# Optimization experiments

Measured on AMD Instinct MI355X. Metric: run time of the kernel, lower is better.

Reference implementation:

```python
import jax, jax.numpy as jnp
import numpy as np
from jax import lax

B, C, H, W = 16, 256, 128, 128
MAX_ROOMS = 10

def _conv(x, w, b):
    y = lax.conv_general_dilated(x, w, window_strides=(1, 1), padding='SAME',
                                 dimension_numbers=('NCHW', 'OIHW', 'NCHW'))
    return y + b[None, :, None, None]

def setup_inputs() -> dict:
    key = jax.random.key(0)
    ks = jax.random.split(key, 16)
    def w(k, shape, fan_in):
        return jax.random.normal(k, shape, jnp.float32) * (1.0 / np.sqrt(fan_in))
    inp = {
        'features': jax.random.normal(ks[0], (B, C, H, W), jnp.float32),
        'conv1_w': w(ks[1], (C // 2, C, 3, 3), C * 9),
        'conv1_b': jnp.zeros((C // 2,), jnp.float32),
        'conv2_w': w(ks[2], (MAX_ROOMS, C // 2, 3, 3), (C // 2) * 9),
        'conv2_b': jnp.zeros((MAX_ROOMS,), jnp.float32),
        'lin1_w': w(ks[3], (256, C * 64), C * 64),
        'lin1_b': jnp.zeros((256,), jnp.float32),
        'lin2_w': w(ks[4], (128, 256), 256),
        'lin2_b': jnp.zeros((128,), jnp.float32),
        'adj1_w': w(ks[5], (64, 256), 256),
        'adj1_b': jnp.zeros((64,), jnp.float32),
        'adj2_w': w(ks[6], (32, 64), 64),
        'adj2_b': jnp.zeros((32,), jnp.float32),
        'adj3_w': w(ks[7], (1, 32), 32),
        'adj3_b': jnp.zeros((1,), jnp.float32),
    }
    return inp

def reference(features, conv1_w, conv1_b, conv2_w, conv2_b,
              lin1_w, lin1_b, lin2_w, lin2_b,
              adj1_w, adj1_b, adj2_w, adj2_b, adj3_w, adj3_b):
    # room detector: conv -> relu -> conv -> sigmoid
    h = jax.nn.relu(_conv(features, conv1_w, conv1_b))
    room_maps = jax.nn.sigmoid(_conv(h, conv2_w, conv2_b))  # [B, max_rooms, H, W]

    # room features: adaptive avg pool to 8x8 (exact since H,W divisible by 8)
    b, c = features.shape[0], features.shape[1]
    pooled = features.reshape(b, c, 8, H // 8, 8, W // 8).mean(axis=(3, 5))  # [B,C,8,8]
    flat = pooled.reshape(b, c * 64)
    feat = jax.nn.relu(flat @ lin1_w.T + lin1_b) @ lin2_w.T + lin2_b  # [B,128]

    # adjacency: original loop uses the SAME pair_feat=cat([feat,feat]) for every (i,j),
    # so compute one prob per batch row and broadcast to all off-diagonal entries.
    pair = jnp.concatenate([feat, feat], axis=-1)  # [B,256]
    a = jax.nn.relu(pair @ adj1_w.T + adj1_b)
    a = jax.nn.relu(a @ adj2_w.T + adj2_b)
    p = jax.nn.sigmoid(a @ adj3_w.T + adj3_b)  # [B,1]
    off_diag = 1.0 - jnp.eye(MAX_ROOMS, dtype=features.dtype)
    adjacency = p[:, :, None] * off_diag[None]  # [B, max_rooms, max_rooms]

    return room_maps, feat, adjacency
```

## Files before the change

### kernel.cpp

```cpp
#include <hip/hip_runtime.h>

#define HH 128
#define WW 128
#define FEAT_OFF 2621440ull
#define ADJ_OFF  2623488ull

typedef __bf16 bf16x8 __attribute__((ext_vector_type(8)));
typedef float  f32x4  __attribute__((ext_vector_type(4)));

__device__ __forceinline__ unsigned short f2bf(float f) {
  unsigned int u = __float_as_uint(f);
  unsigned int r = ((u >> 16) & 1u) + 0x7fffu;
  return (unsigned short)((u + r) >> 16);
}
__device__ __forceinline__ void gl_lds16(const void* g, void* l) {
  __builtin_amdgcn_global_load_lds((const __attribute__((address_space(1))) unsigned int*)g,
                                   (__attribute__((address_space(3))) unsigned int*)l, 16, 0, 0);
}
__device__ __forceinline__ int SW(int r) { return (r ^ (r >> 2)) & 3; }

#define FENCE() asm volatile("" ::: "memory")
#define BARRIER() do { FENCE(); __builtin_amdgcn_s_barrier(); FENCE(); } while (0)
#define LBAR() do { asm volatile("s_waitcnt lgkmcnt(0)" ::: "memory"); __builtin_amdgcn_s_barrier(); FENCE(); } while (0)

__global__ void prep_kernel(const float* __restrict__ w1, const float* __restrict__ w2,
                            unsigned short* __restrict__ W1t, unsigned short* __restrict__ W2t,
                            unsigned short* __restrict__ zp) {
  int id = blockIdx.x * 256 + threadIdx.x;
  if (id < 2048) zp[id] = 0;
  if (id < 294912) {
    int ci = id & 255, co = (id >> 8) & 127, dxy = id >> 15;
    int dy = dxy / 3, dx = dxy - 3 * dy;
    W1t[id] = f2bf(w1[((co * 256 + ci) * 3 + dy) * 3 + dx]);
  }
  if (id < 18432) {
    int ci = id & 127, co = (id >> 7) & 15, dxy = id >> 11;
    int dy = dxy / 3, dx = dxy - 3 * dy;
    W2t[id] = (co < 10) ? f2bf(w2[((co * 128 + ci) * 3 + dy) * 3 + dx]) : (unsigned short)0;
  }
}

__global__ void nhwc_kernel(const float* __restrict__ F, unsigned short* __restrict__ Xn) {
  int t = threadIdx.x, bi = blockIdx.x;
  int x = t & 127;
  int cg = ((bi & 7) << 1) | (t >> 7);
  int y = (bi >> 3) & 127;
  int b = bi >> 10;
  const float* src = F + (((size_t)(b * 256 + cg * 16)) * HH + y) * WW + x;
  __align__(16) unsigned short v[16];
#pragma unroll
  for (int i = 0; i < 16; ++i) v[i] = f2bf(src[(size_t)i * (HH * WW)]);
  unsigned short* dst = Xn + ((((size_t)b * HH + y) * WW) + x) * 256 + cg * 16;
  *(uint4*)dst = *(const uint4*)&v[0];
  *(uint4*)(dst + 8) = *(const uint4*)&v[8];
}

__global__ __launch_bounds__(512) void conv1_kernel(const unsigned short* __restrict__ X,
                                                    const unsigned short* __restrict__ Wt,
                                                    const float* __restrict__ bias,
                                                    unsigned short* __restrict__ Hout,
                                                    const unsigned short* __restrict__ zp) {
  extern __shared__ __align__(16) unsigned short smem[];
  const int t = threadIdx.x, l = t & 63, w = t >> 6;
  int bid = (blockIdx.x & 7) * 128 + (blockIdx.x >> 3);
  const int b = bid >> 6, y0 = (bid & 63) * 2;
  const int ko = l >> 4, r0 = l & 15;
  const int wr = w >> 1, wc = w & 1;
  const int ir = wr >> 1, xoff = (wr & 1) * 64;

  f32x4 acc[4][4];
#pragma unroll
  for (int i = 0; i < 4; ++i)
#pragma unroll
    for (int j = 0; j < 4; ++j) acc[i][j] = {0.f, 0.f, 0.f, 0.f};

  auto stage = [&](int p, int bufsel) {
    int dy = p >> 3, cb = p & 7;
    unsigned short* buf = smem + bufsel * 21504;
    for (int j = w; j < 18; j += 8) {
      int air = (j >= 9) ? 1 : 0;
      int jj = j - air * 9;
      int er = jj * 16 + (l >> 2);
      int xin = er - 1;
      int row = y0 - 1 + dy + air;
      const unsigned short* g;
      if (row >= 0 && row < HH && xin >= 0 && xin < WW && er < 130) {
        int kq = (l & 3) ^ SW(er);
        g = X + (((size_t)b * HH + row) * WW + xin) * 256 + cb * 32 + kq * 8;
      } else g = zp + l * 8;
      gl_lds16(g, buf + j * 512);
    }
    for (int j = w; j < 24; j += 8) {
      int dxi = j >> 3, jj = j & 7;
      int co = jj * 16 + (l >> 2);
      int kq = (l & 3) ^ SW(co);
      gl_lds16(Wt + (((size_t)(dy * 3 + dxi)) * 128 + co) * 256 + cb * 32 + kq * 8,
               buf + 9216 + j * 512);
    }
  };

  stage(0, 0);
  for (int p = 0; p < 24; ++p) {
    if (p < 23) {
      stage(p + 1, (p + 1) & 1);
      FENCE();
      asm volatile("s_waitcnt vmcnt(5)" ::: "memory");
    } else {
      FENCE();
      asm volatile("s_waitcnt vmcnt(0)" ::: "memory");
    }
    BARRIER();
    const unsigned short* buf = smem + (p & 1) * 21504;
    const unsigned short* Ab = buf + ir * 4608;
    const unsigned short* Bb = buf + 9216;
#pragma unroll
    for (int dx = 0; dx < 3; ++dx) {
      bf16x8 a[4], bb[4];
#pragma unroll
      for (int mf = 0; mf < 4; ++mf) {
        int er = xoff + mf * 16 + r0 + dx;
        a[mf] = *(const bf16x8*)(Ab + er * 32 + ((ko ^ SW(er)) << 3));
      }
#pragma unroll
      for (int nf = 0; nf < 4; ++nf) {
        int co = wc * 64 + nf * 16 + r0;
        bb[nf] = *(const bf16x8*)(Bb + dx * 4096 + co * 32 + ((ko ^ SW(co)) << 3));
      }
#pragma unroll
      for (int mf = 0; mf < 4; ++mf)
#pragma unroll
        for (int nf = 0; nf < 4; ++nf)
          acc[mf][nf] = __builtin_amdgcn_mfma_f32_16x16x32_bf16(a[mf], bb[nf], acc[mf][nf], 0, 0, 0);
    }
    BARRIER();
  }

  unsigned short* Ebuf = smem;
  for (int c = 0; c < 4; ++c) {
    if (wr == c) {
#pragma unroll
      for (int nf = 0; nf < 4; ++nf) {
        int col = wc * 64 + nf * 16 + r0;
        float bv = bias[col];
#pragma unroll
        for (int mf = 0; mf < 4; ++mf)
#pragma unroll
          for (int j = 0; j < 4; ++j) {
            int rloc = mf * 16 + (l >> 4) * 4 + j;
            Ebuf[rloc * 128 + col] = f2bf(fmaxf(acc[mf][nf][j] + bv, 0.f));
          }
      }
    }
    LBAR();
    size_t base = (((size_t)b * HH + (y0 + (c >> 1))) * WW + (c & 1) * 64) * 128;
    ((uint4*)(Hout + base))[t] = ((const uint4*)Ebuf)[t];
    ((uint4*)(Hout + base))[t + 512] = ((const uint4*)Ebuf)[t + 512];
    LBAR();
  }
}

__global__ __launch_bounds__(256) void conv2_kernel(const unsigned short* __restrict__ Hn,
                                                    const unsigned short* __restrict__ Wt,
                                                    const float* __restrict__ bias,
                                                    float* __restrict__ rmaps,
                                                    const unsigned short* __restrict__ zp) {
  extern __shared__ __align__(16) unsigned short smem[];
  const int t = threadIdx.x, l = t & 63, w = t >> 6;
  int bid = (blockIdx.x & 7) * 256 + (blockIdx.x >> 3);
  const int b = bid >> 7, y = bid & 127;
  const int ko = l >> 4, r0 = l & 15;

  f32x4 acc[2];
  acc[0] = {0.f, 0.f, 0.f, 0.f};
  acc[1] = {0.f, 0.f, 0.f, 0.f};

  auto stage = [&](int cb, int bufsel) {
    unsigned short* buf = smem + bufsel * 18432;
    for (int j = w; j < 27; j += 4) {
      int rr = (j >= 18) ? 2 : ((j >= 9) ? 1 : 0);
      int jj = j - rr * 9;
      int er = jj * 16 + (l >> 2);
      int xin = er - 1;
      int row = y - 1 + rr;
      const unsigned short* g;
      if (row >= 0 && row < HH && xin >= 0 && xin < WW && er < 130) {
        int kq = (l & 3) ^ SW(er);
        g = Hn + (((size_t)b * HH + row) * WW + xin) * 128 + cb * 32 + kq * 8;
      } else g = zp + l * 8;
      gl_lds16(g, buf + j * 512);
    }
    for (int j = w; j < 9; j += 4) {
      int co = l >> 2;
      int kq = (l & 3) ^ SW(co);
      gl_lds16(Wt + ((size_t)j * 16 + co) * 128 + cb * 32 + kq * 8, buf + 13824 + j * 512);
    }
  };

  stage(0, 0);
  for (int p = 0; p < 4; ++p) {
    if (p < 3) {
      stage(p + 1, (p + 1) & 1);
      FENCE();
      asm volatile("s_waitcnt vmcnt(8)" ::: "memory");
    } else {
      FENCE();
      asm volatile("s_waitcnt vmcnt(0)" ::: "memory");
    }
    BARRIER();
    const unsigned short* buf = smem + (p & 1) * 18432;
#pragma unroll
    for (int dy = 0; dy < 3; ++dy)
#pragma unroll
      for (int dx = 0; dx < 3; ++dx) {
        int tap = dy * 3 + dx;
        bf16x8 bb = *(const bf16x8*)(buf + 13824 + tap * 512 + r0 * 32 + ((ko ^ SW(r0)) << 3));
#pragma unroll
        for (int mf = 0; mf < 2; ++mf) {
          int er = w * 32 + mf * 16 + r0 + dx;
          bf16x8 a = *(const bf16x8*)(buf + dy * 4608 + er * 32 + ((ko ^ SW(er)) << 3));
          acc[mf] = __builtin_amdgcn_mfma_f32_16x16x32_bf16(a, bb, acc[mf], 0, 0, 0);
        }
      }
    BARRIER();
  }

  float* Ef = (float*)smem;
  float bv = (r0 < 10) ? bias[r0] : 0.f;
#pragma unroll
  for (int mf = 0; mf < 2; ++mf)
#pragma unroll
    for (int j = 0; j < 4; ++j) {
      int x = w * 32 + mf * 16 + (l >> 4) * 4 + j;
      Ef[r0 * 128 + x] = 1.f / (1.f + __expf(-(acc[mf][j] + bv)));
    }
  LBAR();
  {
    int co = t >> 5, xi = (t & 31) * 4;
    *(float4*)&rmaps[(((size_t)b * 10 + co) * HH + y) * WW + xi] = *(float4*)&Ef[co * 128 + xi];
    if (t < 64) {
      int idx = t + 256;
      co = idx >> 5; xi = (idx & 31) * 4;
      *(float4*)&rmaps[(((size_t)b * 10 + co) * HH + y) * WW + xi] = *(float4*)&Ef[co * 128 + xi];
    }
  }
}

__global__ void pool2_kernel(const unsigned short* __restrict__ Xn, float* __restrict__ pooled) {
  int t = threadIdx.x, bi = blockIdx.x;
  int b = bi >> 6, py = (bi >> 3) & 7, px = bi & 7;
  int p = t & 127, half = t >> 7;
  float s0 = 0.f, s1 = 0.f;
  const unsigned short* base = Xn + (((size_t)b * HH + py * 16 + half * 8) * WW + px * 16) * 256 + p * 2;
  for (int i = 0; i < 8; ++i)
#pragma unroll
    for (int j = 0; j < 16; ++j) {
      unsigned int v = *(const unsigned int*)(base + ((size_t)i * WW + j) * 256);
      s0 += __uint_as_float(v << 16);
      s1 += __uint_as_float(v & 0xffff0000u);
    }
  __shared__ float red[2][256];
  red[half][p * 2] = s0;
  red[half][p * 2 + 1] = s1;
  __syncthreads();
  float v = red[0][t] + red[1][t];
  pooled[(size_t)b * 16384 + t * 64 + py * 8 + px] = v * (1.f / 256.f);
}

__global__ void lin1_kernel(const float* __restrict__ pooled, const float* __restrict__ w1,
                            const float* __restrict__ b1, float* __restrict__ hidden) {
  int o = blockIdx.x, t = threadIdx.x;
  float acc[16];
#pragma unroll
  for (int b = 0; b < 16; ++b) acc[b] = 0.f;
  const float* wr = w1 + (size_t)o * 16384;
  for (int i = t; i < 16384; i += 256) {
    float wv = wr[i];
#pragma unroll
    for (int b = 0; b < 16; ++b) acc[b] += wv * pooled[(size_t)b * 16384 + i];
  }
  __shared__ float red[16][4];
#pragma unroll
  for (int b = 0; b < 16; ++b) {
    float v = acc[b];
    for (int s = 32; s; s >>= 1) v += __shfl_down(v, s);
    if ((t & 63) == 0) red[b][t >> 6] = v;
  }
  __syncthreads();
  if (t < 16) {
    float v = red[t][0] + red[t][1] + red[t][2] + red[t][3] + b1[o];
    hidden[o * 16 + t] = fmaxf(v, 0.f);
  }
}

__global__ void head_kernel(const float* __restrict__ hidden,
                            const float* __restrict__ w2, const float* __restrict__ b2,
                            const float* __restrict__ a1w, const float* __restrict__ a1b,
                            const float* __restrict__ a2w, const float* __restrict__ a2b,
                            const float* __restrict__ a3w, const float* __restrict__ a3b,
                            float* __restrict__ out) {
  int b = blockIdx.x, t = threadIdx.x;
  __shared__ float hid[256], fs[128], a1[64], a2[32], pv;
  hid[t] = hidden[t * 16 + b];
  __syncthreads();
  if (t < 128) {
    float s = b2[t];
    for (int k = 0; k < 256; ++k) s += hid[k] * w2[t * 256 + k];
    fs[t] = s;
    out[FEAT_OFF + b * 128 + t] = s;
  }
  __syncthreads();
  if (t < 64) {
    float s = a1b[t];
    for (int k = 0; k < 128; ++k) s += fs[k] * (a1w[t * 256 + k] + a1w[t * 256 + 128 + k]);
    a1[t] = fmaxf(s, 0.f);
  }
  __syncthreads();
  if (t < 32) {
    float s = a2b[t];
    for (int k = 0; k < 64; ++k) s += a1[k] * a2w[t * 64 + k];
    a2[t] = fmaxf(s, 0.f);
  }
  __syncthreads();
  if (t == 0) {
    float s = a3b[0];
    for (int k = 0; k < 32; ++k) s += a2[k] * a3w[k];
    pv = 1.f / (1.f + __expf(-s));
  }
  __syncthreads();
  if (t < 100) out[ADJ_OFF + b * 100 + t] = ((t / 10) == (t % 10)) ? 0.f : pv;
}

extern "C" void kernel_launch(void* const* d_in, const int* in_sizes, int n_in,
                              void* d_out, int out_size, void* d_ws, size_t ws_size,
                              hipStream_t stream) {
  const float* F   = (const float*)d_in[0];
  const float* w1  = (const float*)d_in[1];
  const float* b1  = (const float*)d_in[2];
  const float* w2  = (const float*)d_in[3];
  const float* b2  = (const float*)d_in[4];
  const float* l1w = (const float*)d_in[5];
  const float* l1b = (const float*)d_in[6];
  const float* l2w = (const float*)d_in[7];
  const float* l2b = (const float*)d_in[8];
  const float* a1w = (const float*)d_in[9];
  const float* a1b = (const float*)d_in[10];
  const float* a2w = (const float*)d_in[11];
  const float* a2b = (const float*)d_in[12];
  const float* a3w = (const float*)d_in[13];
  const float* a3b = (const float*)d_in[14];
  float* out = (float*)d_out;
  char* ws = (char*)d_ws;

  const size_t zp_off   = 0;
  const size_t w1t_off  = 4096;
  const size_t w2t_off  = w1t_off + 589824;
  const size_t xn_off   = w2t_off + 36864;
  const size_t hn_off   = xn_off + 134217728ull;
  const size_t pool_off = hn_off + 67108864ull;
  const size_t hid_off  = pool_off + 1048576ull;
  const size_t need     = hid_off + 16384ull;
  if (ws_size < need) return;

  unsigned short* zp  = (unsigned short*)(ws + zp_off);
  unsigned short* W1t = (unsigned short*)(ws + w1t_off);
  unsigned short* W2t = (unsigned short*)(ws + w2t_off);
  unsigned short* Xn  = (unsigned short*)(ws + xn_off);
  unsigned short* Hn  = (unsigned short*)(ws + hn_off);
  float* pooled = (float*)(ws + pool_off);
  float* hidden = (float*)(ws + hid_off);

  hipFuncSetAttribute((const void*)conv1_kernel, hipFuncAttributeMaxDynamicSharedMemorySize, 86016);
  hipFuncSetAttribute((const void*)conv2_kernel, hipFuncAttributeMaxDynamicSharedMemorySize, 73728);

  prep_kernel<<<1152, 256, 0, stream>>>(w1, w2, W1t, W2t, zp);
  nhwc_kernel<<<16384, 256, 0, stream>>>(F, Xn);
  pool2_kernel<<<1024, 256, 0, stream>>>(Xn, pooled);
  conv1_kernel<<<1024, 512, 86016, stream>>>(Xn, W1t, b1, Hn, zp);
  conv2_kernel<<<2048, 256, 73728, stream>>>(Hn, W2t, b2, out, zp);
  lin1_kernel<<<256, 256, 0, stream>>>(pooled, l1w, l1b, hidden);
  head_kernel<<<16, 256, 0, stream>>>(hidden, l2w, l2b, a1w, a1b, a2w, a2b, a3w, a3b, out);
}
```

Baseline: 407.7 us.

## Enlarge conv tiles to four rows, and transpose NHWC through LDS

Conv1 now has each block compute four output rows with all 128 output channels, so each wave holds a 64x128 accumulator tile. This reuses each staged input row across more outputs and stages the weights once per four rows instead of once per two. Conv2 likewise processes four rows per block and writes sigmoid outputs straight from registers as float4, skipping the LDS staging. The NHWC conversion now reads with vectorized float4 loads and transposes through a swizzled LDS tile. In exchange, LDS use and accumulator register pressure rise considerably, and fewer blocks are launched, which may reduce occupancy.

```diff
diff --git a/kernel.cpp b/kernel.cpp
--- a/kernel.cpp
+++ b/kernel.cpp
@@ -41,61 +41,77 @@
 }
 
 __global__ void nhwc_kernel(const float* __restrict__ F, unsigned short* __restrict__ Xn) {
+  __shared__ __align__(16) unsigned short tile[16384];
   int t = threadIdx.x, bi = blockIdx.x;
-  int x = t & 127;
-  int cg = ((bi & 7) << 1) | (t >> 7);
-  int y = (bi >> 3) & 127;
-  int b = bi >> 10;
-  const float* src = F + (((size_t)(b * 256 + cg * 16)) * HH + y) * WW + x;
-  __align__(16) unsigned short v[16];
-#pragma unroll
-  for (int i = 0; i < 16; ++i) v[i] = f2bf(src[(size_t)i * (HH * WW)]);
-  unsigned short* dst = Xn + ((((size_t)b * HH + y) * WW) + x) * 256 + cg * 16;
-  *(uint4*)dst = *(const uint4*)&v[0];
-  *(uint4*)(dst + 8) = *(const uint4*)&v[8];
-}
-
-__global__ __launch_bounds__(512) void conv1_kernel(const unsigned short* __restrict__ X,
-                                                    const unsigned short* __restrict__ Wt,
-                                                    const float* __restrict__ bias,
-                                                    unsigned short* __restrict__ Hout,
-                                                    const unsigned short* __restrict__ zp) {
+  int chalf = bi & 1, y = (bi >> 1) & 127, b = bi >> 8;
+  int c0 = chalf * 128;
+  int cp = t >> 2, xq = t & 3;
+  const float* rowA = F + (((size_t)(b * 256 + c0 + cp * 2)) * HH + y) * WW + xq * 32;
+  const float* rowB = rowA + (size_t)HH * WW;
+  unsigned int* tw = (unsigned int*)tile;
+#pragma unroll
+  for (int jj = 0; jj < 8; ++jj) {
+    float4 va = *(const float4*)(rowA + jj * 4);
+    float4 vb = *(const float4*)(rowB + jj * 4);
+    float av[4] = {va.x, va.y, va.z, va.w};
+    float bv[4] = {vb.x, vb.y, vb.z, vb.w};
+#pragma unroll
+    for (int e = 0; e < 4; ++e) {
+      int x = xq * 32 + jj * 4 + e;
+      unsigned int word = (unsigned int)f2bf(av[e]) | ((unsigned int)f2bf(bv[e]) << 16);
+      tw[x * 64 + (((cp >> 2) ^ (x & 15)) << 2) + (cp & 3)] = word;
+    }
+  }
+  __syncthreads();
+  int x = t >> 1, h = t & 1;
+  unsigned short* dst = Xn + ((((size_t)b * HH + y) * WW) + x) * 256 + c0;
+#pragma unroll
+  for (int k = 0; k < 8; ++k) {
+    int s = h * 8 + k;
+    *(uint4*)(dst + s * 8) = *(const uint4*)(tile + x * 128 + ((s ^ (x & 15)) << 3));
+  }
+}
+
+__global__ __launch_bounds__(512, 2) void conv1_kernel(const unsigned short* __restrict__ X,
+                                                       const unsigned short* __restrict__ Wt,
+                                                       const float* __restrict__ bias,
+                                                       unsigned short* __restrict__ Hout,
+                                                       const unsigned short* __restrict__ zp) {
   extern __shared__ __align__(16) unsigned short smem[];
   const int t = threadIdx.x, l = t & 63, w = t >> 6;
-  int bid = (blockIdx.x & 7) * 128 + (blockIdx.x >> 3);
-  const int b = bid >> 6, y0 = (bid & 63) * 2;
+  int bid = (blockIdx.x & 7) * 64 + (blockIdx.x >> 3);
+  const int b = bid >> 5, y0 = (bid & 31) * 4;
   const int ko = l >> 4, r0 = l & 15;
-  const int wr = w >> 1, wc = w & 1;
-  const int ir = wr >> 1, xoff = (wr & 1) * 64;
-
-  f32x4 acc[4][4];
+  const int yloc = w >> 1, xh = w & 1, xoff = xh * 64;
+
+  f32x4 acc[4][8];
 #pragma unroll
   for (int i = 0; i < 4; ++i)
 #pragma unroll
-    for (int j = 0; j < 4; ++j) acc[i][j] = {0.f, 0.f, 0.f, 0.f};
+    for (int j = 0; j < 8; ++j) acc[i][j] = {0.f, 0.f, 0.f, 0.f};
 
   auto stage = [&](int p, int bufsel) {
     int dy = p >> 3, cb = p & 7;
-    unsigned short* buf = smem + bufsel * 21504;
-    for (int j = w; j < 18; j += 8) {
-      int air = (j >= 9) ? 1 : 0;
-      int jj = j - air * 9;
-      int er = jj * 16 + (l >> 2);
-      int xin = er - 1;
-      int row = y0 - 1 + dy + air;
+    unsigned short* buf = smem + bufsel * 30720;
+    for (int c = w; c < 60; c += 8) {
       const unsigned short* g;
-      if (row >= 0 && row < HH && xin >= 0 && xin < WW && er < 130) {
-        int kq = (l & 3) ^ SW(er);
-        g = X + (((size_t)b * HH + row) * WW + xin) * 256 + cb * 32 + kq * 8;
-      } else g = zp + l * 8;
-      gl_lds16(g, buf + j * 512);
-    }
-    for (int j = w; j < 24; j += 8) {
-      int dxi = j >> 3, jj = j & 7;
-      int co = jj * 16 + (l >> 2);
-      int kq = (l & 3) ^ SW(co);
-      gl_lds16(Wt + (((size_t)(dy * 3 + dxi)) * 128 + co) * 256 + cb * 32 + kq * 8,
-               buf + 9216 + j * 512);
+      if (c < 36) {
+        int air = c / 9, jj = c - air * 9;
+        int er = jj * 16 + (l >> 2);
+        int xin = er - 1;
+        int row = y0 - 1 + dy + air;
+        if (row >= 0 && row < HH && xin >= 0 && xin < WW && er < 130) {
+          int kq = (l & 3) ^ SW(er);
+          g = X + (((size_t)b * HH + row) * WW + xin) * 256 + cb * 32 + kq * 8;
+        } else g = zp + l * 8;
+      } else {
+        int cc = c - 36;
+        int dxi = cc >> 3, jj = cc & 7;
+        int co = jj * 16 + (l >> 2);
+        int kq = (l & 3) ^ SW(co);
+        g = Wt + (((size_t)(dy * 3 + dxi)) * 128 + co) * 256 + cb * 32 + kq * 8;
+      }
+      gl_lds16(g, buf + c * 512);
     }
   };
 
@@ -104,57 +120,62 @@
     if (p < 23) {
       stage(p + 1, (p + 1) & 1);
       FENCE();
-      asm volatile("s_waitcnt vmcnt(5)" ::: "memory");
+      asm volatile("s_waitcnt vmcnt(7)" ::: "memory");
     } else {
       FENCE();
       asm volatile("s_waitcnt vmcnt(0)" ::: "memory");
     }
     BARRIER();
-    const unsigned short* buf = smem + (p & 1) * 21504;
-    const unsigned short* Ab = buf + ir * 4608;
-    const unsigned short* Bb = buf + 9216;
+    const unsigned short* buf = smem + (p & 1) * 30720;
+    const unsigned short* Ab = buf + yloc * 4608;
+    const unsigned short* Bb = buf + 18432;
 #pragma unroll
     for (int dx = 0; dx < 3; ++dx) {
-      bf16x8 a[4], bb[4];
+      bf16x8 a[4], bb[8];
 #pragma unroll
       for (int mf = 0; mf < 4; ++mf) {
         int er = xoff + mf * 16 + r0 + dx;
         a[mf] = *(const bf16x8*)(Ab + er * 32 + ((ko ^ SW(er)) << 3));
       }
 #pragma unroll
-      for (int nf = 0; nf < 4; ++nf) {
-        int co = wc * 64 + nf * 16 + r0;
+      for (int nf = 0; nf < 8; ++nf) {
+        int co = nf * 16 + r0;
         bb[nf] = *(const bf16x8*)(Bb + dx * 4096 + co * 32 + ((ko ^ SW(co)) << 3));
       }
 #pragma unroll
       for (int mf = 0; mf < 4; ++mf)
 #pragma unroll
-        for (int nf = 0; nf < 4; ++nf)
+        for (int nf = 0; nf < 8; ++nf)
           acc[mf][nf] = __builtin_amdgcn_mfma_f32_16x16x32_bf16(a[mf], bb[nf], acc[mf][nf], 0, 0, 0);
     }
     BARRIER();
   }
 
-  unsigned short* Ebuf = smem;
-  for (int c = 0; c < 4; ++c) {
-    if (wr == c) {
-#pragma unroll
-      for (int nf = 0; nf < 4; ++nf) {
-        int col = wc * 64 + nf * 16 + r0;
-        float bv = bias[col];
+  unsigned short* E = smem;
+  for (int r = 0; r < 2; ++r) {
+    if (xh == r) {
+#pragma unroll
+      for (int nf = 0; nf < 8; ++nf) {
+        int co = nf * 16 + r0;
+        float bv = bias[co];
 #pragma unroll
         for (int mf = 0; mf < 4; ++mf)
 #pragma unroll
           for (int j = 0; j < 4; ++j) {
-            int rloc = mf * 16 + (l >> 4) * 4 + j;
-            Ebuf[rloc * 128 + col] = f2bf(fmaxf(acc[mf][nf][j] + bv, 0.f));
+            int xl = mf * 16 + ko * 4 + j;
+            E[yloc * 8192 + xl * 128 + co] = f2bf(fmaxf(acc[mf][nf][j] + bv, 0.f));
           }
       }
     }
     LBAR();
-    size_t base = (((size_t)b * HH + (y0 + (c >> 1))) * WW + (c & 1) * 64) * 128;
-    ((uint4*)(Hout + base))[t] = ((const uint4*)Ebuf)[t];
-    ((uint4*)(Hout + base))[t + 512] = ((const uint4*)Ebuf)[t + 512];
+#pragma unroll
+    for (int k = 0; k < 8; ++k) {
+      int idx = k * 512 + t;
+      int yl = idx >> 10, rem = idx & 1023;
+      int xl = rem >> 4, oct = rem & 15;
+      size_t g = (((size_t)b * HH + y0 + yl) * WW + r * 64 + xl) * 128 + oct * 8;
+      *(uint4*)(Hout + g) = ((const uint4*)E)[idx];
+    }
     LBAR();
   }
 }
@@ -166,33 +187,35 @@
                                                     const unsigned short* __restrict__ zp) {
   extern __shared__ __align__(16) unsigned short smem[];
   const int t = threadIdx.x, l = t & 63, w = t >> 6;
-  int bid = (blockIdx.x & 7) * 256 + (blockIdx.x >> 3);
-  const int b = bid >> 7, y = bid & 127;
+  int bid = (blockIdx.x & 7) * 64 + (blockIdx.x >> 3);
+  const int b = bid >> 5, y0 = (bid & 31) * 4;
   const int ko = l >> 4, r0 = l & 15;
-
-  f32x4 acc[2];
-  acc[0] = {0.f, 0.f, 0.f, 0.f};
-  acc[1] = {0.f, 0.f, 0.f, 0.f};
+  const int yloc = w;
+
+  f32x4 acc[8];
+#pragma unroll
+  for (int i = 0; i < 8; ++i) acc[i] = {0.f, 0.f, 0.f, 0.f};
 
   auto stage = [&](int cb, int bufsel) {
-    unsigned short* buf = smem + bufsel * 18432;
-    for (int j = w; j < 27; j += 4) {
-      int rr = (j >= 18) ? 2 : ((j >= 9) ? 1 : 0);
-      int jj = j - rr * 9;
-      int er = jj * 16 + (l >> 2);
-      int xin = er - 1;
-      int row = y - 1 + rr;
+    unsigned short* buf = smem + bufsel * 32256;
+    for (int c = w; c < 63; c += 4) {
       const unsigned short* g;
-      if (row >= 0 && row < HH && xin >= 0 && xin < WW && er < 130) {
-        int kq = (l & 3) ^ SW(er);
-        g = Hn + (((size_t)b * HH + row) * WW + xin) * 128 + cb * 32 + kq * 8;
-      } else g = zp + l * 8;
-      gl_lds16(g, buf + j * 512);
-    }
-    for (int j = w; j < 9; j += 4) {
-      int co = l >> 2;
-      int kq = (l & 3) ^ SW(co);
-      gl_lds16(Wt + ((size_t)j * 16 + co) * 128 + cb * 32 + kq * 8, buf + 13824 + j * 512);
+      if (c < 54) {
+        int air = c / 9, jj = c - air * 9;
+        int er = jj * 16 + (l >> 2);
+        int xin = er - 1;
+        int row = y0 - 1 + air;
+        if (row >= 0 && row < HH && xin >= 0 && xin < WW && er < 130) {
+          int kq = (l & 3) ^ SW(er);
+          g = Hn + (((size_t)b * HH + row) * WW + xin) * 128 + cb * 32 + kq * 8;
+        } else g = zp + l * 8;
+      } else {
+        int tap = c - 54;
+        int co = l >> 2;
+        int kq = (l & 3) ^ SW(co);
+        g = Wt + ((size_t)tap * 16 + co) * 128 + cb * 32 + kq * 8;
+      }
+      gl_lds16(g, buf + c * 512);
     }
   };
 
@@ -201,46 +224,44 @@
     if (p < 3) {
       stage(p + 1, (p + 1) & 1);
       FENCE();
-      asm volatile("s_waitcnt vmcnt(8)" ::: "memory");
+      asm volatile("s_waitcnt vmcnt(15)" ::: "memory");
     } else {
       FENCE();
       asm volatile("s_waitcnt vmcnt(0)" ::: "memory");
     }
     BARRIER();
-    const unsigned short* buf = smem + (p & 1) * 18432;
-#pragma unroll
-    for (int dy = 0; dy < 3; ++dy)
+    const unsigned short* buf = smem + (p & 1) * 32256;
+#pragma unroll
+    for (int dy = 0; dy < 3; ++dy) {
+      const unsigned short* Ab = buf + (yloc + dy) * 4608;
 #pragma unroll
       for (int dx = 0; dx < 3; ++dx) {
         int tap = dy * 3 + dx;
-        bf16x8 bb = *(const bf16x8*)(buf + 13824 + tap * 512 + r0 * 32 + ((ko ^ SW(r0)) << 3));
-#pragma unroll
-        for (int mf = 0; mf < 2; ++mf) {
-          int er = w * 32 + mf * 16 + r0 + dx;
-          bf16x8 a = *(const bf16x8*)(buf + dy * 4608 + er * 32 + ((ko ^ SW(er)) << 3));
-          acc[mf] = __builtin_amdgcn_mfma_f32_16x16x32_bf16(a, bb, acc[mf], 0, 0, 0);
+        bf16x8 bbf = *(const bf16x8*)(buf + (54 + tap) * 512 + r0 * 32 + ((ko ^ SW(r0)) << 3));
+#pragma unroll
+        for (int mf = 0; mf < 8; ++mf) {
+          int er = mf * 16 + r0 + dx;
+          bf16x8 a = *(const bf16x8*)(Ab + er * 32 + ((ko ^ SW(er)) << 3));
+          acc[mf] = __builtin_amdgcn_mfma_f32_16x16x32_bf16(a, bbf, acc[mf], 0, 0, 0);
         }
       }
+    }
     BARRIER();
   }
 
-  float* Ef = (float*)smem;
-  float bv = (r0 < 10) ? bias[r0] : 0.f;
-#pragma unroll
-  for (int mf = 0; mf < 2; ++mf)
-#pragma unroll
-    for (int j = 0; j < 4; ++j) {
-      int x = w * 32 + mf * 16 + (l >> 4) * 4 + j;
-      Ef[r0 * 128 + x] = 1.f / (1.f + __expf(-(acc[mf][j] + bv)));
-    }
-  LBAR();
-  {
-    int co = t >> 5, xi = (t & 31) * 4;
-    *(float4*)&rmaps[(((size_t)b * 10 + co) * HH + y) * WW + xi] = *(float4*)&Ef[co * 128 + xi];
-    if (t < 64) {
-      int idx = t + 256;
-      co = idx >> 5; xi = (idx & 31) * 4;
-      *(float4*)&rmaps[(((size_t)b * 10 + co) * HH + y) * WW + xi] = *(float4*)&Ef[co * 128 + xi];
+  int co = r0;
+  if (co < 10) {
+    float bv = bias[co];
+    int y = y0 + yloc;
+#pragma unroll
+    for (int mf = 0; mf < 8; ++mf) {
+      int x = mf * 16 + ko * 4;
+      float4 o;
+      o.x = 1.f / (1.f + __expf(-(acc[mf][0] + bv)));
+      o.y = 1.f / (1.f + __expf(-(acc[mf][1] + bv)));
+      o.z = 1.f / (1.f + __expf(-(acc[mf][2] + bv)));
+      o.w = 1.f / (1.f + __expf(-(acc[mf][3] + bv)));
+      *(float4*)&rmaps[(((size_t)b * 10 + co) * HH + y) * WW + x] = o;
     }
   }
 }
@@ -369,14 +390,14 @@
   float* pooled = (float*)(ws + pool_off);
   float* hidden = (float*)(ws + hid_off);
 
-  hipFuncSetAttribute((const void*)conv1_kernel, hipFuncAttributeMaxDynamicSharedMemorySize, 86016);
-  hipFuncSetAttribute((const void*)conv2_kernel, hipFuncAttributeMaxDynamicSharedMemorySize, 73728);
+  hipFuncSetAttribute((const void*)conv1_kernel, hipFuncAttributeMaxDynamicSharedMemorySize, 122880);
+  hipFuncSetAttribute((const void*)conv2_kernel, hipFuncAttributeMaxDynamicSharedMemorySize, 129024);
 
   prep_kernel<<<1152, 256, 0, stream>>>(w1, w2, W1t, W2t, zp);
-  nhwc_kernel<<<16384, 256, 0, stream>>>(F, Xn);
+  nhwc_kernel<<<4096, 256, 0, stream>>>(F, Xn);
   pool2_kernel<<<1024, 256, 0, stream>>>(Xn, pooled);
-  conv1_kernel<<<1024, 512, 86016, stream>>>(Xn, W1t, b1, Hn, zp);
-  conv2_kernel<<<2048, 256, 73728, stream>>>(Hn, W2t, b2, out, zp);
+  conv1_kernel<<<512, 512, 122880, stream>>>(Xn, W1t, b1, Hn, zp);
+  conv2_kernel<<<512, 256, 129024, stream>>>(Hn, W2t, b2, out, zp);
   lin1_kernel<<<256, 256, 0, stream>>>(pooled, l1w, l1b, hidden);
   head_kernel<<<16, 256, 0, stream>>>(hidden, l2w, l2b, a1w, a1b, a2w, a2b, a3w, a3b, out);
 }
```

After: 379.6 us. -6.9%, faster.
